# Performance work log

Measured on AMD Instinct MI355X. Metric: run time of the kernel, lower is better.

The kernel has to match this reference:

```python
import jax, jax.numpy as jnp
import numpy as np

ALPHA, BETA, GAMMA, DELTA, EPSILON = 1.0, 0.15, 0.05, 0.0, 0.1
C1 = (0.01 * 255.0) ** 2
C2 = (0.03 * 255.0) ** 2


def _gaussian_kernel11():
    # cv2.getGaussianKernel(11, 1.5) outer product
    g = np.exp(-((np.arange(11) - 5.0) ** 2) / (2.0 * 1.5 ** 2))
    g = g / g.sum()
    return jnp.asarray(np.outer(g, g), dtype=jnp.float32)


def _to_uint8_float(x):
    # clamp to [-1,1], map to [0,1], scale to 255, uint8 truncation (floor)
    x = jnp.clip(x, -1.0, 1.0)
    x01 = jnp.clip((x + 1.0) * 0.5, 0.0, 1.0)
    return jnp.floor(jnp.clip(x01 * 255.0, 0.0, 255.0))


def _depthwise_valid_conv(x, kern2d):
    # x: [B,C,H,W]; 11x11 gaussian, VALID padding == filter2D + [5:-5,5:-5] crop
    C = x.shape[1]
    k = jnp.broadcast_to(kern2d[None, None], (C, 1, 11, 11))
    return jax.lax.conv_general_dilated(
        x, k, window_strides=(1, 1), padding='VALID',
        dimension_numbers=('NCHW', 'OIHW', 'NCHW'), feature_group_count=C)


def _ssim_per_image(img1, img2):
    # img1/img2: [B,C,H,W] floats in [0,255]; basicsr-style SSIM per channel, mean over C
    kern = _gaussian_kernel11()
    conv = lambda t: _depthwise_valid_conv(t, kern)
    mu1, mu2 = conv(img1), conv(img2)
    mu1_sq, mu2_sq, mu1_mu2 = mu1 * mu1, mu2 * mu2, mu1 * mu2
    sigma1_sq = conv(img1 * img1) - mu1_sq
    sigma2_sq = conv(img2 * img2) - mu2_sq
    sigma12 = conv(img1 * img2) - mu1_mu2
    ssim_map = ((2.0 * mu1_mu2 + C1) * (2.0 * sigma12 + C2)) / (
        (mu1_sq + mu2_sq + C1) * (sigma1_sq + sigma2_sq + C2))
    return jnp.mean(ssim_map, axis=(1, 2, 3))  # [B]


def _psnr_per_image(img1, img2):
    mse = jnp.mean((img1 - img2) ** 2, axis=(1, 2, 3))
    psnr = 10.0 * jnp.log10((255.0 ** 2) / jnp.maximum(mse, 1e-12))
    return jnp.where(mse == 0.0, 100.0, psnr)


def setup_inputs() -> dict:
    key = jax.random.key(0)
    k1, k2 = jax.random.split(key)
    shape = (4, 1, 2048, 2048)
    pred = jax.random.normal(k1, shape, dtype=jnp.float32) * 0.5
    target = jax.random.normal(k2, shape, dtype=jnp.float32) * 0.5
    return {"pred": pred, "target": target}


def reference(pred, target):
    # L1 loss
    l1 = jnp.mean(jnp.abs(pred - target))

    # edge-aware gradient loss (finite differences along H and W)
    gx = lambda t: t[:, :, :-1, :] - t[:, :, 1:, :]
    gy = lambda t: t[:, :, :, :-1] - t[:, :, :, 1:]
    grad_loss = (jnp.mean(jnp.abs(gx(pred) - gx(target))) +
                 jnp.mean(jnp.abs(gy(pred) - gy(target))))

    # physical consistency: per-image/channel mean & unbiased std stats + range penalty
    pm = jnp.mean(pred, axis=(2, 3))
    tm = jnp.mean(target, axis=(2, 3))
    energy = jnp.mean((pm - tm) ** 2)
    n = pred.shape[2] * pred.shape[3]
    ps = jnp.sqrt(jnp.sum((pred - pm[:, :, None, None]) ** 2, axis=(2, 3)) / (n - 1))
    ts = jnp.sqrt(jnp.sum((target - tm[:, :, None, None]) ** 2, axis=(2, 3)) / (n - 1))
    dist = jnp.mean((ps - ts) ** 2)
    range_pen = jnp.mean(jax.nn.relu(jnp.abs(pred) - 1.0))
    phys = energy + 0.5 * dist + 0.1 * range_pen

    # SSIM / PSNR on uint8-quantized [0,255] images (metric path, no gradient)
    p8 = _to_uint8_float(pred)
    t8 = _to_uint8_float(target)
    ssim_mean = jnp.clip(jnp.mean(_ssim_per_image(p8, t8)), 0.0, 1.0)
    psnr_mean = jnp.mean(_psnr_per_image(p8, t8))
    ssim_loss = 1.0 - ssim_mean

    total = (ALPHA * l1 + BETA * grad_loss + GAMMA * phys +
             EPSILON * jax.lax.stop_gradient(ssim_loss))
    return total, psnr_mean, ssim_mean
```

## Files before the change

kernel.cpp:

```cpp
#include <hip/hip_runtime.h>
#include <math.h>

#define HDIM 2048
#define WDIM 2048
#define NPIX (HDIM*WDIM)
#define OUTW 2038

#define C1F 6.5025f
#define C2F 58.5225f

constexpr int TH   = 64, TW = 32;
constexpr int IN_R = 80;
constexpr int IN8S = 18;
constexpr int HT_S = 88;
constexpr int NBLK = 8192;

struct GaussW { float g[11]; };

typedef _Float16 half8 __attribute__((ext_vector_type(8)));
typedef float    f32x4 __attribute__((ext_vector_type(4)));

__device__ __forceinline__ float quant_u8f(float x) {
    float c = __builtin_amdgcn_fmed3f(x, -1.0f, 1.0f);
    return truncf((c + 1.0f) * 127.5f);
}
__device__ __forceinline__ float quant_h(float x) {
    float c = __builtin_amdgcn_fmed3f(x, -1.0f, 1.0f);
    return (c + 1.0f) * 127.5f;
}

__device__ __forceinline__ unsigned pk2(float a, float b) {
    return __builtin_bit_cast(unsigned, __builtin_amdgcn_cvt_pkrtz(a, b));
}

__device__ __forceinline__ unsigned pack4_u8(const float* v) {
#if __has_builtin(__builtin_amdgcn_cvt_pk_u8_f32)
    unsigned r = 0;
    r = __builtin_amdgcn_cvt_pk_u8_f32(v[0], 0, r);
    r = __builtin_amdgcn_cvt_pk_u8_f32(v[1], 1, r);
    r = __builtin_amdgcn_cvt_pk_u8_f32(v[2], 2, r);
    r = __builtin_amdgcn_cvt_pk_u8_f32(v[3], 3, r);
    return r;
#else
    return ((unsigned)(int)v[0]) | (((unsigned)(int)v[1]) << 8) |
           (((unsigned)(int)v[2]) << 16) | (((unsigned)(int)v[3]) << 24);
#endif
}

__device__ __forceinline__ half8 unpack_u8x8(unsigned lo, unsigned hi) {
    union { unsigned u[4]; half8 h; } r;
    r.u[0] = pk2((float)(lo & 0xffu),         (float)((lo >> 8)  & 0xffu));
    r.u[1] = pk2((float)((lo >> 16) & 0xffu), (float)((lo >> 24) & 0xffu));
    r.u[2] = pk2((float)(hi & 0xffu),         (float)((hi >> 8)  & 0xffu));
    r.u[3] = pk2((float)((hi >> 16) & 0xffu), (float)((hi >> 24) & 0xffu));
    return r.h;
}

__global__ __launch_bounds__(256) void amsr2_fused(
        const float* __restrict__ pred, const float* __restrict__ targ,
        float* __restrict__ pr, GaussW gw)
{
    __shared__ unsigned Ip8[IN_R * IN8S];
    __shared__ unsigned It8[IN_R * IN8S];
    __shared__ alignas(16) _Float16 HT[5][32 * HT_S];
    __shared__ alignas(16) _Float16 Tg[16 * 32];
    __shared__ float sred[4][10];

    const int b  = blockIdx.z;
    const int r0 = blockIdx.y * TH;
    const int c0 = blockIdx.x * TW;
    const float* pb = pred + (size_t)b * NPIX;
    const float* tb = targ + (size_t)b * NPIX;
    const bool interior = (blockIdx.y < 31) && (blockIdx.x < 63);

    if (threadIdx.x < 16) {
        int n = threadIdx.x;
#pragma unroll
        for (int i = 0; i < 16; ++i) ((unsigned*)Tg)[n * 16 + i] = 0u;
#pragma unroll
        for (int j = 0; j < 11; ++j) Tg[n * 32 + n + j] = (_Float16)gw.g[j];
    }

    float s[9];
#pragma unroll
    for (int c = 0; c < 9; ++c) s[c] = 0.0f;

    if (interior) {
#pragma unroll
        for (int i = 0; i < 2; ++i) {
            int item = threadIdx.x + i * 256;
            int r = item >> 3, d = item & 7;
            const float* prow = pb + (size_t)(r0 + r) * WDIM + (c0 + d * 4);
            const float* trow = tb + (size_t)(r0 + r) * WDIM + (c0 + d * 4);
            float4 a4 = *(const float4*)prow;
            float4 b4 = *(const float4*)trow;
            float4 ad = *(const float4*)(prow + WDIM);
            float4 bd = *(const float4*)(trow + WDIM);
            float p5 = prow[4], t5 = trow[4];
            float pv[4] = {a4.x, a4.y, a4.z, a4.w};
            float tv[4] = {b4.x, b4.y, b4.z, b4.w};
            float pd[4] = {ad.x, ad.y, ad.z, ad.w};
            float td[4] = {bd.x, bd.y, bd.z, bd.w};
            float qp[4], qt[4];
#pragma unroll
            for (int k = 0; k < 4; ++k) { qp[k] = quant_u8f(pv[k]); qt[k] = quant_u8f(tv[k]); }
#pragma unroll
            for (int k = 0; k < 4; ++k) {
                float av = pv[k], bv = tv[k];
                float dd = av - bv;
                s[0] += fabsf(dd);
                s[3] += fmaxf(fabsf(av) - 1.0f, 0.0f);
                s[4] += av;  s[5] += bv;
                s[6] = fmaf(av, av, s[6]);
                s[7] = fmaf(bv, bv, s[7]);
                s[1] += fabsf(dd - (pd[k] - td[k]));
                float nr  = (k < 3) ? pv[k + 1] : p5;
                float nt2 = (k < 3) ? tv[k + 1] : t5;
                s[2] += fabsf(dd - (nr - nt2));
                float qd = qp[k] - qt[k];
                s[8] = fmaf(qd, qd, s[8]);
            }
            Ip8[r * IN8S + d] = pack4_u8(qp);
            It8[r * IN8S + d] = pack4_u8(qt);
        }
        {
            int h = threadIdx.x;
            int r = h >> 2, d = 8 + (h & 3);
            const float* prow = pb + (size_t)(r0 + r) * WDIM + (c0 + d * 4);
            const float* trow = tb + (size_t)(r0 + r) * WDIM + (c0 + d * 4);
            float4 a4 = *(const float4*)prow;
            float4 b4 = *(const float4*)trow;
            float qp[4] = {quant_h(a4.x), quant_h(a4.y), quant_h(a4.z), quant_h(a4.w)};
            float qt[4] = {quant_h(b4.x), quant_h(b4.y), quant_h(b4.z), quant_h(b4.w)};
            Ip8[r * IN8S + d] = pack4_u8(qp);
            It8[r * IN8S + d] = pack4_u8(qt);
        }
        if (threadIdx.x < 192) {
            int h = threadIdx.x;
            int rq = h / 12;
            int r = 64 + rq, d = h - rq * 12;
            const float* prow = pb + (size_t)(r0 + r) * WDIM + (c0 + d * 4);
            const float* trow = tb + (size_t)(r0 + r) * WDIM + (c0 + d * 4);
            float4 a4 = *(const float4*)prow;
            float4 b4 = *(const float4*)trow;
            float qp[4] = {quant_h(a4.x), quant_h(a4.y), quant_h(a4.z), quant_h(a4.w)};
            float qt[4] = {quant_h(b4.x), quant_h(b4.y), quant_h(b4.z), quant_h(b4.w)};
            Ip8[r * IN8S + d] = pack4_u8(qp);
            It8[r * IN8S + d] = pack4_u8(qt);
        }
    } else {
#pragma unroll
        for (int i = 0; i < 2; ++i) {
            int item = threadIdx.x + i * 256;
            int r = item >> 3, d = item & 7;
            int gr = r0 + r, gc = c0 + d * 4;
            const float* prow = pb + (size_t)gr * WDIM + gc;
            const float* trow = tb + (size_t)gr * WDIM + gc;
            float4 a4 = *(const float4*)prow;
            float4 b4 = *(const float4*)trow;
            bool down = gr < (HDIM - 1);
            bool hasR = (gc + 4) < WDIM;
            float4 z4 = make_float4(0.f, 0.f, 0.f, 0.f);
            float4 ad = down ? *(const float4*)(prow + WDIM) : z4;
            float4 bd = down ? *(const float4*)(trow + WDIM) : z4;
            float p5 = hasR ? prow[4] : 0.0f;
            float t5 = hasR ? trow[4] : 0.0f;
            float pv[4] = {a4.x, a4.y, a4.z, a4.w};
            float tv[4] = {b4.x, b4.y, b4.z, b4.w};
            float pd[4] = {ad.x, ad.y, ad.z, ad.w};
            float td[4] = {bd.x, bd.y, bd.z, bd.w};
            float qp[4], qt[4];
#pragma unroll
            for (int k = 0; k < 4; ++k) { qp[k] = quant_u8f(pv[k]); qt[k] = quant_u8f(tv[k]); }
#pragma unroll
            for (int k = 0; k < 4; ++k) {
                float av = pv[k], bv = tv[k];
                float dd = av - bv;
                s[0] += fabsf(dd);
                s[3] += fmaxf(fabsf(av) - 1.0f, 0.0f);
                s[4] += av;  s[5] += bv;
                s[6] = fmaf(av, av, s[6]);
                s[7] = fmaf(bv, bv, s[7]);
                if (down) s[1] += fabsf(dd - (pd[k] - td[k]));
                float nr  = (k < 3) ? pv[k + 1] : p5;
                float nt2 = (k < 3) ? tv[k + 1] : t5;
                if (k < 3 || hasR) s[2] += fabsf(dd - (nr - nt2));
                float qd = qp[k] - qt[k];
                s[8] = fmaf(qd, qd, s[8]);
            }
            Ip8[r * IN8S + d] = pack4_u8(qp);
            It8[r * IN8S + d] = pack4_u8(qt);
        }
#pragma unroll
        for (int ph = 0; ph < 2; ++ph) {
            int r, d;
            bool active = true;
            if (ph == 0) { int h = threadIdx.x; r = h >> 2; d = 8 + (h & 3); }
            else {
                int h = threadIdx.x;
                active = h < 192;
                int rq = h / 12;
                r = 64 + rq; d = h - rq * 12;
            }
            if (active) {
                int gr = r0 + r, gc = c0 + d * 4;
                bool rowok = gr < HDIM;
                const float* prow = pb + (size_t)gr * WDIM + gc;
                const float* trow = tb + (size_t)gr * WDIM + gc;
                float qp[4], qt[4];
                if (rowok && (gc + 3) < WDIM) {
                    float4 a4 = *(const float4*)prow;
                    float4 b4 = *(const float4*)trow;
                    qp[0]=quant_h(a4.x); qp[1]=quant_h(a4.y); qp[2]=quant_h(a4.z); qp[3]=quant_h(a4.w);
                    qt[0]=quant_h(b4.x); qt[1]=quant_h(b4.y); qt[2]=quant_h(b4.z); qt[3]=quant_h(b4.w);
                } else {
#pragma unroll
                    for (int k = 0; k < 4; ++k) {
                        bool ok = rowok && (gc + k) < WDIM;
                        qp[k] = ok ? quant_h(prow[k]) : 0.0f;
                        qt[k] = ok ? quant_h(trow[k]) : 0.0f;
                    }
                }
                Ip8[r * IN8S + d] = pack4_u8(qp);
                It8[r * IN8S + d] = pack4_u8(qt);
            }
        }
    }
    __syncthreads();

    const int lane = threadIdx.x & 63;
    const int wid  = threadIdx.x >> 6;
    const int q    = lane >> 4;
    const int ml   = lane & 15;
    const half8 gfrag = *(const half8*)&Tg[ml * 32 + q * 8];
    const f32x4 zero4 = {0.f, 0.f, 0.f, 0.f};

    for (int pos = wid; pos < 10; pos += 4) {
        int rb = (pos >> 1) * 16;
        int cb = pos & 1;
        int base = (rb + ml) * IN8S + cb * 4 + q * 2;
        unsigned plo = Ip8[base], phi = Ip8[base + 1];
        unsigned tlo = It8[base], thi = It8[base + 1];
        const half8 ap = unpack_u8x8(plo, phi);
        const half8 at = unpack_u8x8(tlo, thi);
        f32x4 d0 = __builtin_amdgcn_mfma_f32_16x16x32_f16(ap,      gfrag, zero4, 0, 0, 0);
        f32x4 d1 = __builtin_amdgcn_mfma_f32_16x16x32_f16(at,      gfrag, zero4, 0, 0, 0);
        f32x4 d2 = __builtin_amdgcn_mfma_f32_16x16x32_f16(ap * ap, gfrag, zero4, 0, 0, 0);
        f32x4 d3 = __builtin_amdgcn_mfma_f32_16x16x32_f16(at * at, gfrag, zero4, 0, 0, 0);
        f32x4 d4 = __builtin_amdgcn_mfma_f32_16x16x32_f16(ap * at, gfrag, zero4, 0, 0, 0);
        int hb = (cb * 16 + ml) * HT_S + rb + q * 4;
        *(uint2*)&HT[0][hb] = make_uint2(pk2(d0[0], d0[1]), pk2(d0[2], d0[3]));
        *(uint2*)&HT[1][hb] = make_uint2(pk2(d1[0], d1[1]), pk2(d1[2], d1[3]));
        *(uint2*)&HT[2][hb] = make_uint2(pk2(d2[0], d2[1]), pk2(d2[2], d2[3]));
        *(uint2*)&HT[3][hb] = make_uint2(pk2(d3[0], d3[1]), pk2(d3[2], d3[3]));
        *(uint2*)&HT[4][hb] = make_uint2(pk2(d4[0], d4[1]), pk2(d4[2], d4[3]));
    }
    __syncthreads();

    float ssum = 0.0f;
    const int th_ = min(TH, OUTW - r0);
    const int tw_ = min(TW, OUTW - c0);
    for (int vp = wid; vp < 8; vp += 4) {
        int rb2 = (vp >> 1) * 16;
        int cb2 = vp & 1;
        f32x4 acc[5];
#pragma unroll
        for (int arr = 0; arr < 5; ++arr) {
            const half8 bf = *(const half8*)&HT[arr][(cb2 * 16 + ml) * HT_S + rb2 + q * 8];
            acc[arr] = __builtin_amdgcn_mfma_f32_16x16x32_f16(gfrag, bf, zero4, 0, 0, 0);
        }
        int col = cb2 * 16 + ml;
#pragma unroll
        for (int reg = 0; reg < 4; ++reg) {
            int row = rb2 + q * 4 + reg;
            if (interior || (row < th_ && col < tw_)) {
                float mu1 = acc[0][reg], mu2 = acc[1][reg];
                float vpp = acc[2][reg], vtt = acc[3][reg], vpt = acc[4][reg];
                float mu1s = mu1 * mu1, mu2s = mu2 * mu2, mu12 = mu1 * mu2;
                float sg1 = vpp - mu1s, sg2 = vtt - mu2s, sg12 = vpt - mu12;
                float num = (2.0f * mu12 + C1F) * (2.0f * sg12 + C2F);
                float den = (mu1s + mu2s + C1F) * (sg1 + sg2 + C2F);
                ssum += num * __builtin_amdgcn_rcpf(den);
            }
        }
    }

    float st10[10];
#pragma unroll
    for (int c = 0; c < 9; ++c) st10[c] = s[c];
    st10[9] = ssum;
#pragma unroll
    for (int c = 0; c < 10; ++c) {
        float v = st10[c];
        for (int off = 32; off > 0; off >>= 1) v += __shfl_down(v, off);
        st10[c] = v;
    }
    if (lane == 0) {
#pragma unroll
        for (int c = 0; c < 10; ++c) sred[wid][c] = st10[c];
    }
    __syncthreads();
    if (threadIdx.x < 10) {
        int c = threadIdx.x;
        int bid = ((b * 32) + blockIdx.y) * 64 + blockIdx.x;
        pr[c * NBLK + bid] = sred[0][c] + sred[1][c] + sred[2][c] + sred[3][c];
    }
}

__global__ __launch_bounds__(256) void amsr2_final(
        const float* __restrict__ pr, float* __restrict__ out)
{
    __shared__ double seg[40];
    int wid = threadIdx.x >> 6, lane = threadIdx.x & 63;
    for (int sidx = wid; sidx < 40; sidx += 4) {
        int c = sidx >> 2, b = sidx & 3;
        const float* base = pr + c * NBLK + b * 2048;
        float4 v[8];
#pragma unroll
        for (int it = 0; it < 8; ++it)
            v[it] = *(const float4*)(base + (it * 64 + lane) * 4);
        double acc = 0.0;
#pragma unroll
        for (int it = 0; it < 8; ++it)
            acc += (double)v[it].x + (double)v[it].y + (double)v[it].z + (double)v[it].w;
        for (int off = 32; off > 0; off >>= 1) acc += __shfl_down(acc, off);
        if (lane == 0) seg[sidx] = acc;
    }
    __syncthreads();
    if (threadIdx.x != 0) return;
    const double n = (double)NPIX;
    double sum0 = 0, sum1 = 0, sum2 = 0, sum3 = 0;
    for (int b = 0; b < 4; ++b) {
        sum0 += seg[0*4+b]; sum1 += seg[1*4+b]; sum2 += seg[2*4+b]; sum3 += seg[3*4+b];
    }
    double l1   = sum0 / (4.0 * n);
    double grad = sum1 / (4.0 * 2047.0 * 2048.0) + sum2 / (4.0 * 2048.0 * 2047.0);
    double energy = 0.0, dist = 0.0, psnr_sum = 0.0, ssim_sum = 0.0;
    for (int b = 0; b < 4; ++b) {
        double Sp  = seg[4*4+b],  St  = seg[5*4+b];
        double Spp = seg[6*4+b],  Stt = seg[7*4+b];
        double Su8 = seg[8*4+b],  Sss = seg[9*4+b];
        double pm = Sp / n, tm = St / n;
        double dm = pm - tm; energy += dm * dm;
        double vp = (Spp - n * pm * pm) / (n - 1.0);
        double vt = (Stt - n * tm * tm) / (n - 1.0);
        double ps = sqrt(fmax(vp, 0.0)), ts = sqrt(fmax(vt, 0.0));
        double dd = ps - ts; dist += dd * dd;
        double mse = Su8 / n;
        double psnr = (mse == 0.0) ? 100.0 : 10.0 * log10(65025.0 / fmax(mse, 1e-12));
        psnr_sum += psnr;
        ssim_sum += Sss / ((double)OUTW * (double)OUTW);
    }
    energy *= 0.25; dist *= 0.25;
    double range_pen = sum3 / (4.0 * n);
    double phys = energy + 0.5 * dist + 0.1 * range_pen;
    double ssim_mean = fmin(fmax(ssim_sum * 0.25, 0.0), 1.0);
    double total = l1 + 0.15 * grad + 0.05 * phys + 0.1 * (1.0 - ssim_mean);
    out[0] = (float)total;
    out[1] = (float)(psnr_sum * 0.25);
    out[2] = (float)ssim_mean;
}

extern "C" void kernel_launch(void* const* d_in, const int* in_sizes, int n_in,
                              void* d_out, int out_size, void* d_ws, size_t ws_size,
                              hipStream_t stream)
{
    (void)in_sizes; (void)n_in; (void)out_size; (void)ws_size;
    const float* pred = (const float*)d_in[0];
    const float* targ = (const float*)d_in[1];
    float* out = (float*)d_out;
    float* pr  = (float*)d_ws;

    GaussW gw;
    {
        double e[11], sm = 0.0;
        for (int i = 0; i < 11; ++i) {
            double d = (double)(i - 5);
            e[i] = exp(-(d * d) / 4.5);
            sm += e[i];
        }
        for (int i = 0; i < 11; ++i) gw.g[i] = (float)(e[i] / sm);
    }

    amsr2_fused<<<dim3(64, 32, 4), 256, 0, stream>>>(pred, targ, pr, gw);
    amsr2_final<<<1, 256, 0, stream>>>(pr, out);
}
```

Baseline: 184.8 us.

## Store quantized tile as fp16 aliased with horizontal-pass buffer to cut LDS

```diff
diff --git a/kernel.cpp b/kernel.cpp
--- a/kernel.cpp
+++ b/kernel.cpp
@@ -11,7 +11,8 @@
 
 constexpr int TH   = 64, TW = 32;
 constexpr int IN_R = 80;
-constexpr int IN8S = 18;
+constexpr int IQ_S = 56;
+constexpr int IQ_H = IN_R * IQ_S;
 constexpr int HT_S = 88;
 constexpr int NBLK = 8192;
 
@@ -24,47 +25,19 @@
     float c = __builtin_amdgcn_fmed3f(x, -1.0f, 1.0f);
     return truncf((c + 1.0f) * 127.5f);
 }
-__device__ __forceinline__ float quant_h(float x) {
-    float c = __builtin_amdgcn_fmed3f(x, -1.0f, 1.0f);
-    return (c + 1.0f) * 127.5f;
-}
 
 __device__ __forceinline__ unsigned pk2(float a, float b) {
     return __builtin_bit_cast(unsigned, __builtin_amdgcn_cvt_pkrtz(a, b));
 }
 
-__device__ __forceinline__ unsigned pack4_u8(const float* v) {
-#if __has_builtin(__builtin_amdgcn_cvt_pk_u8_f32)
-    unsigned r = 0;
-    r = __builtin_amdgcn_cvt_pk_u8_f32(v[0], 0, r);
-    r = __builtin_amdgcn_cvt_pk_u8_f32(v[1], 1, r);
-    r = __builtin_amdgcn_cvt_pk_u8_f32(v[2], 2, r);
-    r = __builtin_amdgcn_cvt_pk_u8_f32(v[3], 3, r);
-    return r;
-#else
-    return ((unsigned)(int)v[0]) | (((unsigned)(int)v[1]) << 8) |
-           (((unsigned)(int)v[2]) << 16) | (((unsigned)(int)v[3]) << 24);
-#endif
-}
-
-__device__ __forceinline__ half8 unpack_u8x8(unsigned lo, unsigned hi) {
-    union { unsigned u[4]; half8 h; } r;
-    r.u[0] = pk2((float)(lo & 0xffu),         (float)((lo >> 8)  & 0xffu));
-    r.u[1] = pk2((float)((lo >> 16) & 0xffu), (float)((lo >> 24) & 0xffu));
-    r.u[2] = pk2((float)(hi & 0xffu),         (float)((hi >> 8)  & 0xffu));
-    r.u[3] = pk2((float)((hi >> 16) & 0xffu), (float)((hi >> 24) & 0xffu));
-    return r.h;
-}
-
-__global__ __launch_bounds__(256) void amsr2_fused(
+__global__ __launch_bounds__(256, 5) void amsr2_fused(
         const float* __restrict__ pred, const float* __restrict__ targ,
         float* __restrict__ pr, GaussW gw)
 {
-    __shared__ unsigned Ip8[IN_R * IN8S];
-    __shared__ unsigned It8[IN_R * IN8S];
-    __shared__ alignas(16) _Float16 HT[5][32 * HT_S];
+    __shared__ alignas(16) _Float16 Ubuf[5 * 32 * HT_S];
     __shared__ alignas(16) _Float16 Tg[16 * 32];
     __shared__ float sred[4][10];
+    _Float16* Iq = Ubuf;
 
     const int b  = blockIdx.z;
     const int r0 = blockIdx.y * TH;
@@ -120,8 +93,10 @@
                 float qd = qp[k] - qt[k];
                 s[8] = fmaf(qd, qd, s[8]);
             }
-            Ip8[r * IN8S + d] = pack4_u8(qp);
-            It8[r * IN8S + d] = pack4_u8(qt);
+            *(uint2*)&Iq[r * IQ_S + d * 4] =
+                make_uint2(pk2(qp[0], qp[1]), pk2(qp[2], qp[3]));
+            *(uint2*)&Iq[IQ_H + r * IQ_S + d * 4] =
+                make_uint2(pk2(qt[0], qt[1]), pk2(qt[2], qt[3]));
         }
         {
             int h = threadIdx.x;
@@ -130,10 +105,12 @@
             const float* trow = tb + (size_t)(r0 + r) * WDIM + (c0 + d * 4);
             float4 a4 = *(const float4*)prow;
             float4 b4 = *(const float4*)trow;
-            float qp[4] = {quant_h(a4.x), quant_h(a4.y), quant_h(a4.z), quant_h(a4.w)};
-            float qt[4] = {quant_h(b4.x), quant_h(b4.y), quant_h(b4.z), quant_h(b4.w)};
-            Ip8[r * IN8S + d] = pack4_u8(qp);
-            It8[r * IN8S + d] = pack4_u8(qt);
+            float qp[4] = {quant_u8f(a4.x), quant_u8f(a4.y), quant_u8f(a4.z), quant_u8f(a4.w)};
+            float qt[4] = {quant_u8f(b4.x), quant_u8f(b4.y), quant_u8f(b4.z), quant_u8f(b4.w)};
+            *(uint2*)&Iq[r * IQ_S + d * 4] =
+                make_uint2(pk2(qp[0], qp[1]), pk2(qp[2], qp[3]));
+            *(uint2*)&Iq[IQ_H + r * IQ_S + d * 4] =
+                make_uint2(pk2(qt[0], qt[1]), pk2(qt[2], qt[3]));
         }
         if (threadIdx.x < 192) {
             int h = threadIdx.x;
@@ -143,10 +120,12 @@
             const float* trow = tb + (size_t)(r0 + r) * WDIM + (c0 + d * 4);
             float4 a4 = *(const float4*)prow;
             float4 b4 = *(const float4*)trow;
-            float qp[4] = {quant_h(a4.x), quant_h(a4.y), quant_h(a4.z), quant_h(a4.w)};
-            float qt[4] = {quant_h(b4.x), quant_h(b4.y), quant_h(b4.z), quant_h(b4.w)};
-            Ip8[r * IN8S + d] = pack4_u8(qp);
-            It8[r * IN8S + d] = pack4_u8(qt);
+            float qp[4] = {quant_u8f(a4.x), quant_u8f(a4.y), quant_u8f(a4.z), quant_u8f(a4.w)};
+            float qt[4] = {quant_u8f(b4.x), quant_u8f(b4.y), quant_u8f(b4.z), quant_u8f(b4.w)};
+            *(uint2*)&Iq[r * IQ_S + d * 4] =
+                make_uint2(pk2(qp[0], qp[1]), pk2(qp[2], qp[3]));
+            *(uint2*)&Iq[IQ_H + r * IQ_S + d * 4] =
+                make_uint2(pk2(qt[0], qt[1]), pk2(qt[2], qt[3]));
         }
     } else {
 #pragma unroll
@@ -188,8 +167,10 @@
                 float qd = qp[k] - qt[k];
                 s[8] = fmaf(qd, qd, s[8]);
             }
-            Ip8[r * IN8S + d] = pack4_u8(qp);
-            It8[r * IN8S + d] = pack4_u8(qt);
+            *(uint2*)&Iq[r * IQ_S + d * 4] =
+                make_uint2(pk2(qp[0], qp[1]), pk2(qp[2], qp[3]));
+            *(uint2*)&Iq[IQ_H + r * IQ_S + d * 4] =
+                make_uint2(pk2(qt[0], qt[1]), pk2(qt[2], qt[3]));
         }
 #pragma unroll
         for (int ph = 0; ph < 2; ++ph) {
@@ -211,18 +192,20 @@
                 if (rowok && (gc + 3) < WDIM) {
                     float4 a4 = *(const float4*)prow;
                     float4 b4 = *(const float4*)trow;
-                    qp[0]=quant_h(a4.x); qp[1]=quant_h(a4.y); qp[2]=quant_h(a4.z); qp[3]=quant_h(a4.w);
-                    qt[0]=quant_h(b4.x); qt[1]=quant_h(b4.y); qt[2]=quant_h(b4.z); qt[3]=quant_h(b4.w);
+                    qp[0]=quant_u8f(a4.x); qp[1]=quant_u8f(a4.y); qp[2]=quant_u8f(a4.z); qp[3]=quant_u8f(a4.w);
+                    qt[0]=quant_u8f(b4.x); qt[1]=quant_u8f(b4.y); qt[2]=quant_u8f(b4.z); qt[3]=quant_u8f(b4.w);
                 } else {
 #pragma unroll
                     for (int k = 0; k < 4; ++k) {
                         bool ok = rowok && (gc + k) < WDIM;
-                        qp[k] = ok ? quant_h(prow[k]) : 0.0f;
-                        qt[k] = ok ? quant_h(trow[k]) : 0.0f;
+                        qp[k] = ok ? quant_u8f(prow[k]) : 0.0f;
+                        qt[k] = ok ? quant_u8f(trow[k]) : 0.0f;
                     }
                 }
-                Ip8[r * IN8S + d] = pack4_u8(qp);
-                It8[r * IN8S + d] = pack4_u8(qt);
+                *(uint2*)&Iq[r * IQ_S + d * 4] =
+                    make_uint2(pk2(qp[0], qp[1]), pk2(qp[2], qp[3]));
+                *(uint2*)&Iq[IQ_H + r * IQ_S + d * 4] =
+                    make_uint2(pk2(qt[0], qt[1]), pk2(qt[2], qt[3]));
             }
         }
     }
@@ -235,25 +218,41 @@
     const half8 gfrag = *(const half8*)&Tg[ml * 32 + q * 8];
     const f32x4 zero4 = {0.f, 0.f, 0.f, 0.f};
 
-    for (int pos = wid; pos < 10; pos += 4) {
-        int rb = (pos >> 1) * 16;
-        int cb = pos & 1;
-        int base = (rb + ml) * IN8S + cb * 4 + q * 2;
-        unsigned plo = Ip8[base], phi = Ip8[base + 1];
-        unsigned tlo = It8[base], thi = It8[base + 1];
-        const half8 ap = unpack_u8x8(plo, phi);
-        const half8 at = unpack_u8x8(tlo, thi);
-        f32x4 d0 = __builtin_amdgcn_mfma_f32_16x16x32_f16(ap,      gfrag, zero4, 0, 0, 0);
-        f32x4 d1 = __builtin_amdgcn_mfma_f32_16x16x32_f16(at,      gfrag, zero4, 0, 0, 0);
-        f32x4 d2 = __builtin_amdgcn_mfma_f32_16x16x32_f16(ap * ap, gfrag, zero4, 0, 0, 0);
-        f32x4 d3 = __builtin_amdgcn_mfma_f32_16x16x32_f16(at * at, gfrag, zero4, 0, 0, 0);
-        f32x4 d4 = __builtin_amdgcn_mfma_f32_16x16x32_f16(ap * at, gfrag, zero4, 0, 0, 0);
-        int hb = (cb * 16 + ml) * HT_S + rb + q * 4;
-        *(uint2*)&HT[0][hb] = make_uint2(pk2(d0[0], d0[1]), pk2(d0[2], d0[3]));
-        *(uint2*)&HT[1][hb] = make_uint2(pk2(d1[0], d1[1]), pk2(d1[2], d1[3]));
-        *(uint2*)&HT[2][hb] = make_uint2(pk2(d2[0], d2[1]), pk2(d2[2], d2[3]));
-        *(uint2*)&HT[3][hb] = make_uint2(pk2(d3[0], d3[1]), pk2(d3[2], d3[3]));
-        *(uint2*)&HT[4][hb] = make_uint2(pk2(d4[0], d4[1]), pk2(d4[2], d4[3]));
+    const int npos = (wid < 2) ? 3 : 2;
+    half8 hap[3], hat[3];
+#pragma unroll
+    for (int i = 0; i < 3; ++i) {
+        if (i < npos) {
+            int pos = wid + i * 4;
+            int rb = (pos >> 1) * 16;
+            int cb = pos & 1;
+            int base = (rb + ml) * IQ_S + cb * 16 + q * 8;
+            hap[i] = *(const half8*)&Iq[base];
+            hat[i] = *(const half8*)&Iq[IQ_H + base];
+        }
+    }
+    __syncthreads();
+
+#pragma unroll
+    for (int i = 0; i < 3; ++i) {
+        if (i < npos) {
+            int pos = wid + i * 4;
+            int rb = (pos >> 1) * 16;
+            int cb = pos & 1;
+            const half8 ap = hap[i];
+            const half8 at = hat[i];
+            f32x4 d0 = __builtin_amdgcn_mfma_f32_16x16x32_f16(ap,      gfrag, zero4, 0, 0, 0);
+            f32x4 d1 = __builtin_amdgcn_mfma_f32_16x16x32_f16(at,      gfrag, zero4, 0, 0, 0);
+            f32x4 d2 = __builtin_amdgcn_mfma_f32_16x16x32_f16(ap * ap, gfrag, zero4, 0, 0, 0);
+            f32x4 d3 = __builtin_amdgcn_mfma_f32_16x16x32_f16(at * at, gfrag, zero4, 0, 0, 0);
+            f32x4 d4 = __builtin_amdgcn_mfma_f32_16x16x32_f16(ap * at, gfrag, zero4, 0, 0, 0);
+            int hb = (cb * 16 + ml) * HT_S + rb + q * 4;
+            *(uint2*)&Ubuf[0 * 32 * HT_S + hb] = make_uint2(pk2(d0[0], d0[1]), pk2(d0[2], d0[3]));
+            *(uint2*)&Ubuf[1 * 32 * HT_S + hb] = make_uint2(pk2(d1[0], d1[1]), pk2(d1[2], d1[3]));
+            *(uint2*)&Ubuf[2 * 32 * HT_S + hb] = make_uint2(pk2(d2[0], d2[1]), pk2(d2[2], d2[3]));
+            *(uint2*)&Ubuf[3 * 32 * HT_S + hb] = make_uint2(pk2(d3[0], d3[1]), pk2(d3[2], d3[3]));
+            *(uint2*)&Ubuf[4 * 32 * HT_S + hb] = make_uint2(pk2(d4[0], d4[1]), pk2(d4[2], d4[3]));
+        }
     }
     __syncthreads();
 
@@ -266,7 +265,8 @@
         f32x4 acc[5];
 #pragma unroll
         for (int arr = 0; arr < 5; ++arr) {
-            const half8 bf = *(const half8*)&HT[arr][(cb2 * 16 + ml) * HT_S + rb2 + q * 8];
+            const half8 bf = *(const half8*)&Ubuf[arr * 32 * HT_S +
+                                                  (cb2 * 16 + ml) * HT_S + rb2 + q * 8];
             acc[arr] = __builtin_amdgcn_mfma_f32_16x16x32_f16(gfrag, bf, zero4, 0, 0, 0);
         }
         int col = cb2 * 16 + ml;
```

New measurement: 177.8 us. 3.8% less time.
